# Optimization experiments

Hardware: AMD Instinct MI355X
Metric: run time of the kernel (lower is better)

Reference implementation:

```python
import jax, jax.numpy as jnp
import numpy as np

NUM_HEADS = 16

def _stablemax3_s(x):
    # 3rd-order Taylor approx of exp(x), Eq 38
    pos = 1.0 + x * (1.0 + 0.5 * x * (1.0 + x / 3.0))
    neg = 1.0 / (1.0 - x * (1.0 - 0.5 * x * (1.0 - x / 3.0)))
    return jnp.where(x >= 0, pos, neg)

def stablemax3(logits, axis=-1):
    logits = logits - jnp.max(logits, axis=axis, keepdims=True)
    s = _stablemax3_s(logits)
    return s / jnp.sum(s, axis=axis, keepdims=True)

def setup_inputs() -> dict:
    key = jax.random.key(0)
    k1, k2, k3 = jax.random.split(key, 3)
    B, S, D = 2, 2048, 1024
    x = jax.random.normal(k1, (B, S, D), dtype=jnp.float32)
    w_qkv = jax.random.normal(k2, (3 * D, D), dtype=jnp.float32) * 0.02
    w_out = jax.random.normal(k3, (D, D), dtype=jnp.float32) * 0.02
    b_out = jnp.zeros((D,), dtype=jnp.float32)
    return {"x": x, "w_qkv": w_qkv, "w_out": w_out, "b_out": b_out}

def reference(x, w_qkv, w_out, b_out):
    B, S, D = x.shape
    H = NUM_HEADS
    hd = D // H
    scale = hd ** (-0.5)
    qkv = x @ w_qkv.T                                  # [B, S, 3D]
    qkv = qkv.reshape(B, S, 3, H, hd)
    qkv = jnp.transpose(qkv, (2, 0, 3, 1, 4))          # [3, B, H, S, hd]
    q, k, v = qkv[0], qkv[1], qkv[2]                   # pos(.) is identity here
    attn = jnp.einsum('bhsd,bhtd->bhst', q, k) * scale # [B, H, S, S]
    attn = stablemax3(attn, axis=-1)
    out = jnp.einsum('bhst,bhtd->bhsd', attn, v)       # [B, H, S, hd]
    out = jnp.transpose(out, (0, 2, 1, 3)).reshape(B, S, D)
    return out @ w_out.T + b_out
```

## Files before the change

kernel.cpp:

```cpp
#include <hip/hip_runtime.h>

typedef _Float16 half8 __attribute__((ext_vector_type(8)));
typedef _Float16 half4 __attribute__((ext_vector_type(4)));
typedef _Float16 half2v __attribute__((ext_vector_type(2)));
typedef float floatx4 __attribute__((ext_vector_type(4)));
typedef unsigned int uint2v __attribute__((ext_vector_type(2)));
typedef unsigned int uint4v __attribute__((ext_vector_type(4)));

__device__ __forceinline__ void gl_lds16(const _Float16* g, _Float16* l) {
    __builtin_amdgcn_global_load_lds(
        (const __attribute__((address_space(1))) void*)g,
        (__attribute__((address_space(3))) void*)l, 16, 0, 0);
}

__device__ __forceinline__ half2v cvt_pk(float a, float b) {
    return __builtin_bit_cast(half2v, __builtin_amdgcn_cvt_pkrtz(a, b));
}

__device__ __forceinline__ half2v rcp2(half2v d) {
#if __has_builtin(__builtin_amdgcn_rcph)
    half2v r;
    r[0] = __builtin_amdgcn_rcph(d[0]);
    r[1] = __builtin_amdgcn_rcph(d[1]);
    return r;
#else
    half2v r;
    r[0] = (_Float16)__builtin_amdgcn_rcpf((float)d[0]);
    r[1] = (_Float16)__builtin_amdgcn_rcpf((float)d[1]);
    return r;
#endif
}

__device__ __forceinline__ float dot2acc(half2v a, float acc) {
#if __has_builtin(__builtin_amdgcn_fdot2)
    const half2v one = {(_Float16)1.0f, (_Float16)1.0f};
    return __builtin_amdgcn_fdot2(a, one, acc, false);
#else
    return acc + (float)a[0] + (float)a[1];
#endif
}

__device__ __forceinline__ half8 from4(half2v a, half2v b, half2v c, half2v d) {
    uint4v u = {__builtin_bit_cast(unsigned int, a), __builtin_bit_cast(unsigned int, b),
                __builtin_bit_cast(unsigned int, c), __builtin_bit_cast(unsigned int, d)};
    return __builtin_bit_cast(half8, u);
}

__device__ __forceinline__ half8 from_lohi(half4 lo, half4 hi) {
    uint2v l = __builtin_bit_cast(uint2v, lo);
    uint2v h = __builtin_bit_cast(uint2v, hi);
    uint4v u = {l[0], l[1], h[0], h[1]};
    return __builtin_bit_cast(half8, u);
}

__global__ __launch_bounds__(256) void cvt_xw(const floatx4* __restrict__ x,
                                              const floatx4* __restrict__ wq,
                                              half4* __restrict__ xh,
                                              half4* __restrict__ wqh) {
    int i = blockIdx.x * 256 + threadIdx.x;
    floatx4 v;
    half4 h;
    if (i < 1048576) {
        v = x[i];
#pragma unroll
        for (int j = 0; j < 4; ++j) h[j] = (_Float16)v[j];
        xh[i] = h;
    } else {
        int j4 = i - 1048576;
        v = wq[j4];
#pragma unroll
        for (int j = 0; j < 4; ++j) h[j] = (_Float16)v[j];
        wqh[j4] = h;
    }
}

__global__ __launch_bounds__(256) void cvt_f32_f16(const floatx4* __restrict__ in,
                                                   half4* __restrict__ out, int n4) {
    int i = blockIdx.x * 256 + threadIdx.x;
    if (i >= n4) return;
    floatx4 v = in[i];
    half4 h;
#pragma unroll
    for (int j = 0; j < 4; ++j) h[j] = (_Float16)v[j];
    out[i] = h;
}

__global__ __launch_bounds__(256) void gemm_qkv(const _Float16* __restrict__ A,
                                                const _Float16* __restrict__ B,
                                                _Float16* __restrict__ qh,
                                                _Float16* __restrict__ kh,
                                                _Float16* __restrict__ vth) {
    const int K = 1024;
    __shared__ _Float16 SH[128 * 68];
    _Float16* As = SH;
    _Float16* Bs = SH + 4096;
    const int t = threadIdx.x;
    const int lane = t & 63, w = t >> 6;
    const int l15 = lane & 15, quad = lane >> 4;
    const int wm = w >> 1, wn = w & 1;
    const int m0 = blockIdx.y * 128, n0 = blockIdx.x * 128;

    floatx4 acc[4][4];
    const floatx4 zf = {0.f, 0.f, 0.f, 0.f};
#pragma unroll
    for (int i = 0; i < 4; ++i)
#pragma unroll
        for (int j = 0; j < 4; ++j) acc[i][j] = zf;

    for (int kt = 0; kt < K; kt += 32) {
        __syncthreads();
#pragma unroll
        for (int it = 0; it < 2; ++it) {
            int cc = it * 256 + t;
            int row = cc >> 2, kc = cc & 3;
            gl_lds16(&A[(size_t)(m0 + row) * K + kt + kc * 8], &As[cc * 8]);
            gl_lds16(&B[(size_t)(n0 + row) * K + kt + kc * 8], &Bs[cc * 8]);
        }
        __syncthreads();
        half8 af[4], bfr[4];
#pragma unroll
        for (int i = 0; i < 4; ++i)
            af[i] = *(const half8*)&As[(wm * 64 + i * 16 + l15) * 32 + quad * 8];
#pragma unroll
        for (int i = 0; i < 4; ++i)
            bfr[i] = *(const half8*)&Bs[(wn * 64 + i * 16 + l15) * 32 + quad * 8];
#pragma unroll
        for (int mi = 0; mi < 4; ++mi)
#pragma unroll
            for (int ni = 0; ni < 4; ++ni)
                acc[mi][ni] = __builtin_amdgcn_mfma_f32_16x16x32_f16(af[mi], bfr[ni],
                                                                     acc[mi][ni], 0, 0, 0);
    }

    const int b = m0 >> 11, s0 = m0 & 2047;
#pragma unroll
    for (int hf = 0; hf < 2; ++hf) {
        __syncthreads();
        if (wn == hf) {
#pragma unroll
            for (int mi = 0; mi < 4; ++mi)
#pragma unroll
                for (int ni = 0; ni < 4; ++ni)
#pragma unroll
                    for (int r = 0; r < 4; ++r)
                        SH[(wm * 64 + mi * 16 + quad * 4 + r) * 68 + ni * 16 + l15] =
                            (_Float16)acc[mi][ni][r];
        }
        __syncthreads();
        const int cbase = n0 + hf * 64;
        if (n0 < 2048) {
            const int hh = (cbase & 1023) >> 6;
            _Float16* dst = (n0 < 1024 ? qh : kh) + (size_t)((b << 4) | hh) * 131072;
#pragma unroll
            for (int it = 0; it < 4; ++it) {
                int cc = it * 256 + t;
                int r = cc >> 3, c8 = cc & 7;
                half4 lo = *(const half4*)&SH[r * 68 + c8 * 8];
                half4 hi = *(const half4*)&SH[r * 68 + c8 * 8 + 4];
                *(half8*)&dst[(size_t)(s0 + r) * 64 + c8 * 8] = from_lohi(lo, hi);
            }
        } else {
            const int hh = (cbase - 2048) >> 6;
            _Float16* dst = vth + (size_t)((b << 4) | hh) * 131072;
#pragma unroll
            for (int it = 0; it < 4; ++it) {
                int cc = it * 256 + t;
                int d = cc >> 4, s8 = cc & 15;
                half8 v;
#pragma unroll
                for (int j = 0; j < 8; ++j) v[j] = SH[(s8 * 8 + j) * 68 + d];
                *(half8*)&dst[(size_t)d * 2048 + s0 + s8 * 8] = v;
            }
        }
    }
}

__global__ __launch_bounds__(256) void gemm_out(const _Float16* __restrict__ A,
                                                const _Float16* __restrict__ B,
                                                float* __restrict__ C,
                                                const float* __restrict__ bias) {
    const int K = 1024, N = 1024;
    __shared__ _Float16 SH[6144];
    _Float16* As = SH;
    _Float16* Bs = SH + 2048;
    const int t = threadIdx.x;
    const int lane = t & 63, w = t >> 6;
    const int l15 = lane & 15, quad = lane >> 4;
    const int wm = w >> 1, wn = w & 1;
    const int m0 = blockIdx.y * 64, n0 = blockIdx.x * 128;

    floatx4 acc[2][4];
    const floatx4 zf = {0.f, 0.f, 0.f, 0.f};
#pragma unroll
    for (int i = 0; i < 2; ++i)
#pragma unroll
        for (int j = 0; j < 4; ++j) acc[i][j] = zf;

    for (int kt = 0; kt < K; kt += 32) {
        __syncthreads();
        {
            int row = t >> 2, kc = t & 3;
            gl_lds16(&A[(size_t)(m0 + row) * K + kt + kc * 8], &As[t * 8]);
        }
#pragma unroll
        for (int it = 0; it < 2; ++it) {
            int cc = it * 256 + t;
            int row = cc >> 2, kc = cc & 3;
            gl_lds16(&B[(size_t)(n0 + row) * K + kt + kc * 8], &Bs[cc * 8]);
        }
        __syncthreads();
        half8 af[2], bfr[4];
#pragma unroll
        for (int i = 0; i < 2; ++i)
            af[i] = *(const half8*)&As[(wm * 32 + i * 16 + l15) * 32 + quad * 8];
#pragma unroll
        for (int i = 0; i < 4; ++i)
            bfr[i] = *(const half8*)&Bs[(wn * 64 + i * 16 + l15) * 32 + quad * 8];
#pragma unroll
        for (int mi = 0; mi < 2; ++mi)
#pragma unroll
            for (int ni = 0; ni < 4; ++ni)
                acc[mi][ni] = __builtin_amdgcn_mfma_f32_16x16x32_f16(af[mi], bfr[ni],
                                                                     acc[mi][ni], 0, 0, 0);
    }

#pragma unroll
    for (int mi = 0; mi < 2; ++mi) {
#pragma unroll
        for (int ni = 0; ni < 4; ++ni) {
            int col = n0 + wn * 64 + ni * 16 + l15;
            float bv = bias[col];
#pragma unroll
            for (int r = 0; r < 4; ++r) {
                int row = m0 + wm * 32 + mi * 16 + quad * 4 + r;
                C[(size_t)row * N + col] = acc[mi][ni][r] + bv;
            }
        }
    }
}

__global__ __launch_bounds__(256, 4) void attn_kernel(const _Float16* __restrict__ qh,
                                                      const _Float16* __restrict__ kh,
                                                      const _Float16* __restrict__ vth,
                                                      _Float16* __restrict__ out) {
    __shared__ _Float16 SM[16384];

    const int t = threadIdx.x;
    const int lane = t & 63, w = t >> 6;
    const int l15 = lane & 15, quad = lane >> 4;
    const int sw = l15 & 7;
    const int qg = w >> 1, kg = w & 1;
    const int q0 = blockIdx.x * 64;
    const int bh = blockIdx.y;
    const int b = bh >> 4, h = bh & 15;

    const _Float16* Qp = qh + (size_t)bh * 131072 + q0 * 64;
    const _Float16* Kp = kh + (size_t)bh * 131072;
    const _Float16* VTp = vth + (size_t)bh * 131072;

    const int row0 = t >> 3, cg0 = (t & 7) ^ (row0 & 7);
    const _Float16* K0 = &Kp[(size_t)row0 * 64 + cg0 * 8];
    const _Float16* K1 = &Kp[(size_t)(32 + row0) * 64 + cg0 * 8];
    const _Float16* V0 = &VTp[(size_t)row0 * 2048 + cg0 * 8];
    const _Float16* V1 = &VTp[(size_t)(32 + row0) * 2048 + cg0 * 8];

    const floatx4 zf = {0.f, 0.f, 0.f, 0.f};

    half8 qf[2][2];
#pragma unroll
    for (int nh = 0; nh < 2; ++nh)
#pragma unroll
        for (int kk = 0; kk < 2; ++kk) {
            half8 q = *(const half8*)&Qp[(qg * 32 + nh * 16 + l15) * 64 + kk * 32 + quad * 8];
#pragma unroll
            for (int j = 0; j < 8; ++j) q[j] = q[j] * (_Float16)0.125f;
            qf[nh][kk] = q;
        }

    float rmax[2] = {-1.0e30f, -1.0e30f};
    gl_lds16(K0, &SM[t * 8]);
    gl_lds16(K1, &SM[2048 + t * 8]);
    __syncthreads();
    for (int kt = 0, cur = 0; kt < 2048; kt += 64, cur ^= 1) {
        if (kt + 64 < 2048) {
            _Float16* kd = cur ? &SM[0] : &SM[4096];
            gl_lds16(K0 + (size_t)(kt + 64) * 64, kd + t * 8);
            gl_lds16(K1 + (size_t)(kt + 64) * 64, kd + 2048 + t * 8);
        }
        const _Float16* Ks = cur ? &SM[4096] : &SM[0];
        floatx4 sa[2][2];
#pragma unroll
        for (int Ti = 0; Ti < 2; ++Ti) { sa[Ti][0] = zf; sa[Ti][1] = zf; }
#pragma unroll
        for (int kk = 0; kk < 2; ++kk) {
            half8 kf[2];
#pragma unroll
            for (int Ti = 0; Ti < 2; ++Ti)
                kf[Ti] = *(const half8*)&Ks[(((kg * 2 + Ti) * 16 + l15) << 6) +
                                            ((((kk << 2) + quad) ^ sw) << 3)];
            __builtin_amdgcn_s_setprio(1);
#pragma unroll
            for (int Ti = 0; Ti < 2; ++Ti)
#pragma unroll
                for (int nh = 0; nh < 2; ++nh)
                    sa[Ti][nh] = __builtin_amdgcn_mfma_f32_16x16x32_f16(kf[Ti], qf[nh][kk],
                                                                        sa[Ti][nh], 0, 0, 0);
            __builtin_amdgcn_s_setprio(0);
        }
#pragma unroll
        for (int Ti = 0; Ti < 2; ++Ti)
#pragma unroll
            for (int nh = 0; nh < 2; ++nh)
#pragma unroll
                for (int r = 0; r < 4; ++r)
                    rmax[nh] = fmaxf(rmax[nh], sa[Ti][nh][r]);
        __syncthreads();
    }
#pragma unroll
    for (int nh = 0; nh < 2; ++nh) {
        rmax[nh] = fmaxf(rmax[nh], __shfl_xor(rmax[nh], 16, 64));
        rmax[nh] = fmaxf(rmax[nh], __shfl_xor(rmax[nh], 32, 64));
    }
    {
        float* EXM = (float*)SM;
        if (quad == 0) {
#pragma unroll
            for (int nh = 0; nh < 2; ++nh)
                EXM[((qg * 2 + nh) * 2 + kg) * 16 + l15] = rmax[nh];
        }
        __syncthreads();
#pragma unroll
        for (int nh = 0; nh < 2; ++nh)
            rmax[nh] = fmaxf(EXM[((qg * 2 + nh) * 2 + 0) * 16 + l15],
                             EXM[((qg * 2 + nh) * 2 + 1) * 16 + l15]);
        __syncthreads();
    }
    const floatx4 xmv[2] = {{-rmax[0], -rmax[0], -rmax[0], -rmax[0]},
                            {-rmax[1], -rmax[1], -rmax[1], -rmax[1]}};

    const half2v cA = {(_Float16)(-1.0f / 6.0f), (_Float16)(-1.0f / 6.0f)};
    const half2v cB = {(_Float16)0.5f, (_Float16)0.5f};
    const half2v cC = {(_Float16)-1.0f, (_Float16)-1.0f};
    const half2v cD = {(_Float16)1.0f, (_Float16)1.0f};

    float rsum[2] = {0.f, 0.f};
    floatx4 oacc[4][2];
#pragma unroll
    for (int i = 0; i < 4; ++i) { oacc[i][0] = zf; oacc[i][1] = zf; }

    gl_lds16(K0, &SM[t * 8]);
    gl_lds16(K1, &SM[2048 + t * 8]);
    gl_lds16(V0, &SM[8192 + t * 8]);
    gl_lds16(V1, &SM[8192 + 2048 + t * 8]);
    __syncthreads();
    for (int kt = 0, cur = 0; kt < 2048; kt += 64, cur ^= 1) {
        if (kt + 64 < 2048) {
            _Float16* kd = cur ? &SM[0] : &SM[4096];
            _Float16* vd = cur ? &SM[8192] : &SM[12288];
            gl_lds16(K0 + (size_t)(kt + 64) * 64, kd + t * 8);
            gl_lds16(K1 + (size_t)(kt + 64) * 64, kd + 2048 + t * 8);
            gl_lds16(V0 + (kt + 64), vd + t * 8);
            gl_lds16(V1 + (kt + 64), vd + 2048 + t * 8);
        }
        const _Float16* Ks = cur ? &SM[4096] : &SM[0];
        const _Float16* VTs = cur ? &SM[12288] : &SM[8192];

        floatx4 sa[2][2];
#pragma unroll
        for (int Ti = 0; Ti < 2; ++Ti) { sa[Ti][0] = xmv[0]; sa[Ti][1] = xmv[1]; }
#pragma unroll
        for (int kk = 0; kk < 2; ++kk) {
            half8 kf[2];
#pragma unroll
            for (int Ti = 0; Ti < 2; ++Ti)
                kf[Ti] = *(const half8*)&Ks[(((kg * 2 + Ti) * 16 + l15) << 6) +
                                            ((((kk << 2) + quad) ^ sw) << 3)];
            __builtin_amdgcn_s_setprio(1);
#pragma unroll
            for (int Ti = 0; Ti < 2; ++Ti)
#pragma unroll
                for (int nh = 0; nh < 2; ++nh)
                    sa[Ti][nh] = __builtin_amdgcn_mfma_f32_16x16x32_f16(kf[Ti], qf[nh][kk],
                                                                        sa[Ti][nh], 0, 0, 0);
            __builtin_amdgcn_s_setprio(0);
        }
        half8 vf[4];
#pragma unroll
        for (int di = 0; di < 4; ++di) {
            const int bl = (di * 16 + l15) << 6;
            const int clo = (((kg << 2) + (quad >> 1)) ^ sw) << 3;
            const int chi = (((kg << 2) + 2 + (quad >> 1)) ^ sw) << 3;
            half4 lo = *(const half4*)&VTs[bl + clo + ((quad & 1) << 2)];
            half4 hi = *(const half4*)&VTs[bl + chi + ((quad & 1) << 2)];
            vf[di] = from_lohi(lo, hi);
        }
#pragma unroll
        for (int nh = 0; nh < 2; ++nh) {
            half2v p2m[4];
#pragma unroll
            for (int m = 0; m < 4; ++m) {
                int Ti = m >> 1;
                int r0 = (m & 1) * 2;
                half2v x2 = cvt_pk(sa[Ti][nh][r0], sa[Ti][nh][r0 + 1]);
                half2v hp = __builtin_elementwise_fma(x2, cA, cB);
                hp = __builtin_elementwise_fma(x2, hp, cC);
                hp = __builtin_elementwise_fma(x2, hp, cD);
                half2v p2 = rcp2(hp);
                rsum[nh] = dot2acc(p2, rsum[nh]);
                p2m[m] = p2;
            }
            half8 pb = from4(p2m[0], p2m[1], p2m[2], p2m[3]);
            __builtin_amdgcn_s_setprio(1);
#pragma unroll
            for (int di = 0; di < 4; ++di)
                oacc[di][nh] = __builtin_amdgcn_mfma_f32_16x16x32_f16(vf[di], pb,
                                                                      oacc[di][nh], 0, 0, 0);
            __builtin_amdgcn_s_setprio(0);
        }
        __syncthreads();
    }

#pragma unroll
    for (int nh = 0; nh < 2; ++nh) {
        rsum[nh] += __shfl_xor(rsum[nh], 16, 64);
        rsum[nh] += __shfl_xor(rsum[nh], 32, 64);
    }

    float* EXO = (float*)SM;
    float* EXS = (float*)(SM + 8192);
    _Float16* Os = SM + 8320;
    if (kg) {
#pragma unroll
        for (int nh = 0; nh < 2; ++nh)
#pragma unroll
            for (int di = 0; di < 4; ++di)
                *(floatx4*)&EXO[(((((qg * 2 + nh) * 4 + di) * 4 + quad) * 16) + l15) * 4] =
                    oacc[di][nh];
        if (quad == 0) {
#pragma unroll
            for (int nh = 0; nh < 2; ++nh)
                EXS[(qg * 2 + nh) * 16 + l15] = rsum[nh];
        }
    }
    __syncthreads();
    if (!kg) {
        float inv[2];
#pragma unroll
        for (int nh = 0; nh < 2; ++nh)
            inv[nh] = 1.0f / (rsum[nh] + EXS[(qg * 2 + nh) * 16 + l15]);
#pragma unroll
        for (int nh = 0; nh < 2; ++nh)
#pragma unroll
            for (int di = 0; di < 4; ++di) {
                floatx4 part = *(const floatx4*)
                    &EXO[(((((qg * 2 + nh) * 4 + di) * 4 + quad) * 16) + l15) * 4];
                half4 hv;
#pragma unroll
                for (int r = 0; r < 4; ++r)
                    hv[r] = (_Float16)((oacc[di][nh][r] + part[r]) * inv[nh]);
                *(half4*)&Os[(qg * 32 + nh * 16 + l15) * 72 + di * 16 + quad * 4] = hv;
            }
    }
    __syncthreads();
    _Float16* Op = out + (size_t)(b * 2048 + q0) * 1024 + h * 64;
#pragma unroll
    for (int it = 0; it < 2; ++it) {
        int cc = it * 256 + t;
        int r = cc >> 3, c8 = cc & 7;
        *(half8*)&Op[(size_t)r * 1024 + c8 * 8] = *(const half8*)&Os[r * 72 + c8 * 8];
    }
}

extern "C" void kernel_launch(void* const* d_in, const int* in_sizes, int n_in,
                              void* d_out, int out_size, void* d_ws, size_t ws_size,
                              hipStream_t stream) {
    const float* x_f = (const float*)d_in[0];
    const float* wqkv_f = (const float*)d_in[1];
    const float* wout_f = (const float*)d_in[2];
    const float* bias_f = (const float*)d_in[3];

    char* ws = (char*)d_ws;
    _Float16* xh = (_Float16*)(ws);
    _Float16* aoh = xh;
    _Float16* wqh = (_Float16*)(ws + 8388608);
    _Float16* woh = wqh;
    _Float16* qh = (_Float16*)(ws + 14680064);
    _Float16* kh = (_Float16*)(ws + 23068672);
    _Float16* vth = (_Float16*)(ws + 31457280);

    cvt_xw<<<7168, 256, 0, stream>>>((const floatx4*)x_f, (const floatx4*)wqkv_f,
                                     (half4*)xh, (half4*)wqh);
    gemm_qkv<<<dim3(24, 32), 256, 0, stream>>>(xh, wqh, qh, kh, vth);
    cvt_f32_f16<<<1024, 256, 0, stream>>>((const floatx4*)wout_f, (half4*)woh, 262144);
    attn_kernel<<<dim3(32, 32), 256, 0, stream>>>(qh, kh, vth, aoh);
    gemm_out<<<dim3(8, 64), 256, 0, stream>>>(aoh, woh, (float*)d_out, bias_f);
}
```

Baseline: 213.1 us.

## Load K fragments directly from global into registers instead of via LDS

K tiles are no longer staged through shared memory. Each wave now reads its own K fragments straight from global memory into registers, with a register double-buffer that prefetches the next tile. This removes the per-iteration barrier in the max pass and halves the LDS traffic in the main pass, which now stages only V. The cost is higher register pressure and redundant global reads, since each wave reloads K rows that another wave shares, leaning on L2/L1 cache hits and exposing global latency if prefetch is insufficient.

```diff
diff --git a/kernel.cpp b/kernel.cpp
--- a/kernel.cpp
+++ b/kernel.cpp
@@ -258,9 +258,9 @@
     const _Float16* Kp = kh + (size_t)bh * 131072;
     const _Float16* VTp = vth + (size_t)bh * 131072;
 
+    const _Float16* Kl = Kp + (kg * 32 + l15) * 64 + quad * 8;
+
     const int row0 = t >> 3, cg0 = (t & 7) ^ (row0 & 7);
-    const _Float16* K0 = &Kp[(size_t)row0 * 64 + cg0 * 8];
-    const _Float16* K1 = &Kp[(size_t)(32 + row0) * 64 + cg0 * 8];
     const _Float16* V0 = &VTp[(size_t)row0 * 2048 + cg0 * 8];
     const _Float16* V1 = &VTp[(size_t)(32 + row0) * 2048 + cg0 * 8];
 
@@ -278,43 +278,67 @@
         }
 
     float rmax[2] = {-1.0e30f, -1.0e30f};
-    gl_lds16(K0, &SM[t * 8]);
-    gl_lds16(K1, &SM[2048 + t * 8]);
-    __syncthreads();
-    for (int kt = 0, cur = 0; kt < 2048; kt += 64, cur ^= 1) {
-        if (kt + 64 < 2048) {
-            _Float16* kd = cur ? &SM[0] : &SM[4096];
-            gl_lds16(K0 + (size_t)(kt + 64) * 64, kd + t * 8);
-            gl_lds16(K1 + (size_t)(kt + 64) * 64, kd + 2048 + t * 8);
-        }
-        const _Float16* Ks = cur ? &SM[4096] : &SM[0];
-        floatx4 sa[2][2];
-#pragma unroll
-        for (int Ti = 0; Ti < 2; ++Ti) { sa[Ti][0] = zf; sa[Ti][1] = zf; }
-#pragma unroll
-        for (int kk = 0; kk < 2; ++kk) {
-            half8 kf[2];
+    {
+        half8 ka[2][2], kb[2][2];
+#pragma unroll
+        for (int Ti = 0; Ti < 2; ++Ti)
+#pragma unroll
+            for (int kk = 0; kk < 2; ++kk)
+                ka[Ti][kk] = *(const half8*)&Kl[Ti * 1024 + kk * 32];
+        for (int kt = 0; kt < 2048; kt += 128) {
 #pragma unroll
             for (int Ti = 0; Ti < 2; ++Ti)
-                kf[Ti] = *(const half8*)&Ks[(((kg * 2 + Ti) * 16 + l15) << 6) +
-                                            ((((kk << 2) + quad) ^ sw) << 3)];
+#pragma unroll
+                for (int kk = 0; kk < 2; ++kk)
+                    kb[Ti][kk] = *(const half8*)&Kl[(size_t)(kt + 64) * 64 + Ti * 1024 + kk * 32];
+            floatx4 sa[2][2];
+#pragma unroll
+            for (int Ti = 0; Ti < 2; ++Ti) { sa[Ti][0] = zf; sa[Ti][1] = zf; }
             __builtin_amdgcn_s_setprio(1);
 #pragma unroll
+            for (int kk = 0; kk < 2; ++kk)
+#pragma unroll
+                for (int Ti = 0; Ti < 2; ++Ti)
+#pragma unroll
+                    for (int nh = 0; nh < 2; ++nh)
+                        sa[Ti][nh] = __builtin_amdgcn_mfma_f32_16x16x32_f16(ka[Ti][kk], qf[nh][kk],
+                                                                            sa[Ti][nh], 0, 0, 0);
+            __builtin_amdgcn_s_setprio(0);
+#pragma unroll
             for (int Ti = 0; Ti < 2; ++Ti)
 #pragma unroll
                 for (int nh = 0; nh < 2; ++nh)
-                    sa[Ti][nh] = __builtin_amdgcn_mfma_f32_16x16x32_f16(kf[Ti], qf[nh][kk],
-                                                                        sa[Ti][nh], 0, 0, 0);
+#pragma unroll
+                    for (int r = 0; r < 4; ++r)
+                        rmax[nh] = fmaxf(rmax[nh], sa[Ti][nh][r]);
+            if (kt + 128 < 2048) {
+#pragma unroll
+                for (int Ti = 0; Ti < 2; ++Ti)
+#pragma unroll
+                    for (int kk = 0; kk < 2; ++kk)
+                        ka[Ti][kk] = *(const half8*)&Kl[(size_t)(kt + 128) * 64 + Ti * 1024 + kk * 32];
+            }
+            floatx4 sb[2][2];
+#pragma unroll
+            for (int Ti = 0; Ti < 2; ++Ti) { sb[Ti][0] = zf; sb[Ti][1] = zf; }
+            __builtin_amdgcn_s_setprio(1);
+#pragma unroll
+            for (int kk = 0; kk < 2; ++kk)
+#pragma unroll
+                for (int Ti = 0; Ti < 2; ++Ti)
+#pragma unroll
+                    for (int nh = 0; nh < 2; ++nh)
+                        sb[Ti][nh] = __builtin_amdgcn_mfma_f32_16x16x32_f16(kb[Ti][kk], qf[nh][kk],
+                                                                            sb[Ti][nh], 0, 0, 0);
             __builtin_amdgcn_s_setprio(0);
-        }
-#pragma unroll
-        for (int Ti = 0; Ti < 2; ++Ti)
-#pragma unroll
-            for (int nh = 0; nh < 2; ++nh)
-#pragma unroll
-                for (int r = 0; r < 4; ++r)
-                    rmax[nh] = fmaxf(rmax[nh], sa[Ti][nh][r]);
-        __syncthreads();
+#pragma unroll
+            for (int Ti = 0; Ti < 2; ++Ti)
+#pragma unroll
+                for (int nh = 0; nh < 2; ++nh)
+#pragma unroll
+                    for (int r = 0; r < 4; ++r)
+                        rmax[nh] = fmaxf(rmax[nh], sb[Ti][nh][r]);
+        }
     }
 #pragma unroll
     for (int nh = 0; nh < 2; ++nh) {
@@ -348,42 +372,43 @@
 #pragma unroll
     for (int i = 0; i < 4; ++i) { oacc[i][0] = zf; oacc[i][1] = zf; }
 
-    gl_lds16(K0, &SM[t * 8]);
-    gl_lds16(K1, &SM[2048 + t * 8]);
-    gl_lds16(V0, &SM[8192 + t * 8]);
-    gl_lds16(V1, &SM[8192 + 2048 + t * 8]);
+    gl_lds16(V0, &SM[t * 8]);
+    gl_lds16(V1, &SM[2048 + t * 8]);
+    half8 ka[2][2];
+#pragma unroll
+    for (int Ti = 0; Ti < 2; ++Ti)
+#pragma unroll
+        for (int kk = 0; kk < 2; ++kk)
+            ka[Ti][kk] = *(const half8*)&Kl[Ti * 1024 + kk * 32];
     __syncthreads();
+
     for (int kt = 0, cur = 0; kt < 2048; kt += 64, cur ^= 1) {
         if (kt + 64 < 2048) {
-            _Float16* kd = cur ? &SM[0] : &SM[4096];
-            _Float16* vd = cur ? &SM[8192] : &SM[12288];
-            gl_lds16(K0 + (size_t)(kt + 64) * 64, kd + t * 8);
-            gl_lds16(K1 + (size_t)(kt + 64) * 64, kd + 2048 + t * 8);
+            _Float16* vd = cur ? &SM[0] : &SM[4096];
             gl_lds16(V0 + (kt + 64), vd + t * 8);
             gl_lds16(V1 + (kt + 64), vd + 2048 + t * 8);
         }
-        const _Float16* Ks = cur ? &SM[4096] : &SM[0];
-        const _Float16* VTs = cur ? &SM[12288] : &SM[8192];
-
         floatx4 sa[2][2];
 #pragma unroll
         for (int Ti = 0; Ti < 2; ++Ti) { sa[Ti][0] = xmv[0]; sa[Ti][1] = xmv[1]; }
-#pragma unroll
-        for (int kk = 0; kk < 2; ++kk) {
-            half8 kf[2];
+        __builtin_amdgcn_s_setprio(1);
+#pragma unroll
+        for (int kk = 0; kk < 2; ++kk)
 #pragma unroll
             for (int Ti = 0; Ti < 2; ++Ti)
-                kf[Ti] = *(const half8*)&Ks[(((kg * 2 + Ti) * 16 + l15) << 6) +
-                                            ((((kk << 2) + quad) ^ sw) << 3)];
-            __builtin_amdgcn_s_setprio(1);
+#pragma unroll
+                for (int nh = 0; nh < 2; ++nh)
+                    sa[Ti][nh] = __builtin_amdgcn_mfma_f32_16x16x32_f16(ka[Ti][kk], qf[nh][kk],
+                                                                        sa[Ti][nh], 0, 0, 0);
+        __builtin_amdgcn_s_setprio(0);
+        if (kt + 64 < 2048) {
 #pragma unroll
             for (int Ti = 0; Ti < 2; ++Ti)
 #pragma unroll
-                for (int nh = 0; nh < 2; ++nh)
-                    sa[Ti][nh] = __builtin_amdgcn_mfma_f32_16x16x32_f16(kf[Ti], qf[nh][kk],
-                                                                        sa[Ti][nh], 0, 0, 0);
-            __builtin_amdgcn_s_setprio(0);
-        }
+                for (int kk = 0; kk < 2; ++kk)
+                    ka[Ti][kk] = *(const half8*)&Kl[(size_t)(kt + 64) * 64 + Ti * 1024 + kk * 32];
+        }
+        const _Float16* VTs = cur ? &SM[4096] : &SM[0];
         half8 vf[4];
 #pragma unroll
         for (int di = 0; di < 4; ++di) {
```

Result: slower. 263.9 us (+23.9%).
